# Kernel optimization log

Hardware: AMD Instinct MI355X
Metric: run time of the kernel (lower is better)

## Reference

```python
import jax, jax.numpy as jnp
import numpy as np

# 5x5 Sobel kernels (exact constants from the torch module)
_GX5 = np.array([[2.,1.,1e-6,-1.,-2.],[3.,2.,1e-6,-2.,-3.],[4.,3.,0.,-3.,-4.],[3.,2.,1e-6,-2.,-3.],[2.,1.,1e-6,-1.,-2.]], np.float32)
_GY5 = np.array([[2.,3.,4.,3.,2.],[1.,2.,3.,2.,1.],[1e-6,1e-6,1e-6,1e-6,1e-6],[-1.,-2.,-3.,-2.,-1.],[-2.,-3.,-4.,-3.,-2.]], np.float32)


def _sobel(x):  # x: [B,1,H,W] -> [B,2,H,W] (gx, gy)
    k = jnp.stack([jnp.asarray(_GX5), jnp.asarray(_GY5)])[:, None]  # [2,1,5,5]
    return jax.lax.conv_general_dilated(x, k, (1, 1), 'SAME',
                                        dimension_numbers=('NCHW', 'OIHW', 'NCHW'))


def _quantize(gx, gy):
    # OrientQuantize: magnitude + orientation quantized to 8 bins
    div = 3.1416 / 8.0
    mag = jnp.sqrt(gx * gx + gy * gy + 1e-8)
    o = jnp.arctan2(gy, gx)
    conds = [
        (o >= div) & (o < 3 * div),
        (o >= 3 * div) & (o < 5 * div),
        (o >= 5 * div) & (o < 7 * div),
        ((o >= 7 * div) & (o < 8 * div)) | ((o >= -8 * div) & (o < -7 * div)),
        (o >= -7 * div) & (o < -5 * div),
        (o >= -5 * div) & (o < -3 * div),
        (o >= -3 * div) & (o < -div),
        (o >= -div) & (o < div),
    ]
    q = jnp.select(conds, [jnp.full_like(o, float(i)) for i in range(8)], 3.0)
    return mag, q.astype(jnp.int32)


def setup_inputs() -> dict:
    key = jax.random.key(0)
    k1, k2, k3 = jax.random.split(key, 3)
    return {
        'seg_map': jax.random.normal(k1, (2, 21, 256, 256), jnp.float32),
        'dense_ft': jax.random.normal(k2, (2, 256, 256, 256), jnp.float32),
        'mask': jax.random.normal(k3, (2, 21, 256, 256), jnp.float32),
        'label_with_bg': jnp.ones((2, 21), jnp.float32),
    }


def reference(seg_map, dense_ft, mask, label_with_bg):
    BETA, K, STEP = 1000.0, 100, 5
    n, C, h, w = seg_map.shape
    nfg, ch, hw = C - 1, dense_ft.shape[1], h * w

    # ---- Mix_fg: per-class Sobel orientation edges on sharpened softmax ----
    seg = jax.nn.softmax(seg_map * BETA, axis=1)[:, 1:]            # [n,nfg,h,w]
    edges = _sobel(seg.reshape(n * nfg, 1, h, w)).reshape(n, nfg, 2, h, w)
    label_fg = label_with_bg[:, 1:]                                 # [n,nfg]
    edges = edges * label_fg[:, :, None, None, None]
    mag, q = _quantize(edges[:, :, 0], edges[:, :, 1])              # [n,nfg,h,w]

    # ---- boundary pixels: strongest-K edge magnitudes per (b,c) ----
    _, pos = jax.lax.top_k(mag.reshape(n, nfg, hw), K)              # [n,nfg,K]
    o = jnp.take_along_axis(q.reshape(n, nfg, hw), pos, -1) + 1     # 1..8

    # ---- in_out_div: walk STEP pixels along/against gradient orientation ----
    mod4 = ((o % 4) == 0).astype(jnp.int32)
    horiz = ((o == 2) | (o == 6)).astype(jnp.int32)
    p_out = jnp.where(o < 4, STEP * STEP, -STEP)   # (-STEP)**(1+(o<4))
    p_in = jnp.where(o < 4, -STEP, 1)              # (-STEP)**(o<4)
    s_out = jnp.where(o % 2 == 0, -1, 1)           # (-1)**(1+o)
    s_in = -s_out                                   # (-1)**o
    out_idx = pos + p_out * mod4 * w + s_out * horiz
    in_idx = pos + p_in * mod4 * w + s_in * horiz

    def valid(x):
        return (x % (w - 1) != 0) & (x % (w - 1) != 1) & (x > 0) & (x < hw - 1)

    v_out, v_in = valid(out_idx), valid(in_idx)                     # [n,nfg,K] bool
    oi = jnp.clip(out_idx, 0, hw - 1)
    ii = jnp.clip(in_idx, 0, hw - 1)

    # ---- gather features / mask probs at walked positions ----
    dense = jax.nn.softmax(dense_ft, axis=1).reshape(n, ch, hw)
    msk = jax.nn.softmax(mask, axis=1).reshape(n, C, hw)
    b = jnp.arange(n)[:, None, None]
    outs = dense[b, :, oi]                                          # [n,nfg,K,ch]
    ins = jax.lax.stop_gradient(dense[b, :, ii])                    # detached
    outs_m = jax.lax.stop_gradient(msk[b, :, oi])
    ins_m = jax.lax.stop_gradient(msk[b, :, ii])

    sim = jnp.einsum('bcie,bcje->bcij', outs, ins)                  # [n,nfg,K,K]
    sim_m = jnp.einsum('bcie,bcje->bcij', outs_m, ins_m)

    fvi = v_in.astype(sim.dtype)
    fvo = v_out.astype(sim.dtype)
    ci = jnp.maximum(fvi.sum(-1), 1.0)
    co = jnp.maximum(fvo.sum(-1), 1.0)

    def rowmean(s):  # mean over in-samples -> [n,nfg,K]
        return (s * fvi[:, :, None, :]).sum(-1) / ci[..., None]

    def colmean(s):  # mean over out-samples -> [n,nfg,K]
        return (s * fvo[:, :, :, None]).sum(-2) / co[..., None]

    def gmean(s):    # global masked mean -> [n,nfg]
        num = (s * fvo[:, :, :, None] * fvi[:, :, None, :]).sum((-2, -1))
        return num / jnp.maximum(fvo.sum(-1) * fvi.sum(-1), 1.0)

    def beacon(sgn_mask, sgn_dense, vals, v):
        # loss_constructor: signed masked means over FP/FN/TP/TN categories
        def term(cat, sign):
            m = (cat & v).astype(vals.dtype)
            cnt = m.sum(-1)
            return sign * jnp.where(cnt > 0, (vals * m).sum(-1) / jnp.maximum(cnt, 1.0), 0.0)
        FP = sgn_mask & ~sgn_dense
        FN = ~sgn_mask & sgn_dense
        TP = ~sgn_mask & ~sgn_dense
        TN = sgn_mask & sgn_dense
        return term(FP, -1.0) + term(FN, 1.0) + term(TP, 1.0) + term(TN, -1.0)

    g = gmean(sim)
    gm = gmean(sim_m)
    rm, rmm = rowmean(sim), rowmean(sim_m)
    cm, cmm = colmean(sim), colmean(sim_m)
    sgn_rm = jax.lax.stop_gradient(rm) > g[..., None]
    sgn_rmm = rmm > gm[..., None]
    sgn_cm = jax.lax.stop_gradient(cm) > g[..., None]
    sgn_cmm = cmm > gm[..., None]

    loss_bc = beacon(sgn_rmm, sgn_rm, rm, v_out) + beacon(sgn_cmm, sgn_cm, cm, v_in)
    gate = ((v_in.sum(-1) >= 10) & (v_out.sum(-1) >= 10)).astype(loss_bc.dtype)
    gate = gate * (label_fg > 0).astype(loss_bc.dtype)
    return (loss_bc * gate).sum()
```

## Files before the change

### kernel.cpp

```cpp
#include <hip/hip_runtime.h>
#include <math.h>

#define HW 65536
#define WID 256
#define HEI 256
#define NB 2
#define NFG 20
#define NMAP 40
#define CH 256
#define CSEG 21
#define TK 100
#define PARTS 32
#define PARTN (HW / PARTS)
#define RPP (HEI / PARTS)
#define CAND (PARTS * TK)
#define MCH 13

__device__ __constant__ float c_GX[25] = {
  2.f,1.f,1e-6f,-1.f,-2.f,
  3.f,2.f,1e-6f,-2.f,-3.f,
  4.f,3.f,0.f,-3.f,-4.f,
  3.f,2.f,1e-6f,-2.f,-3.f,
  2.f,1.f,1e-6f,-1.f,-2.f};
__device__ __constant__ float c_GY[25] = {
  2.f,3.f,4.f,3.f,2.f,
  1.f,2.f,3.f,2.f,1.f,
  1e-6f,1e-6f,1e-6f,1e-6f,1e-6f,
  -1.f,-2.f,-3.f,-2.f,-1.f,
  -2.f,-3.f,-4.f,-3.f,-2.f};

__global__ __launch_bounds__(256) void k_seg(const float* __restrict__ seg_map,
                                             double* __restrict__ seg) {
  int idx = blockIdx.x * blockDim.x + threadIdx.x;
  if (idx >= NB * HW) return;
  int b = idx / HW, p = idx % HW;
  double x[CSEG];
  double m = -INFINITY;
  #pragma unroll
  for (int c = 0; c < CSEG; ++c) {
    double v = (double)seg_map[(size_t)(b * CSEG + c) * HW + p] * 1000.0;
    x[c] = v;
    m = fmax(m, v);
  }
  double s = 0.0;
  #pragma unroll
  for (int c = 0; c < CSEG; ++c) {
    double d = x[c] - m;
    double e = (d < -746.0) ? 0.0 : exp(d);
    x[c] = e; s += e;
  }
  #pragma unroll
  for (int c = 1; c < CSEG; ++c)
    seg[(size_t)(b * NFG + (c - 1)) * HW + p] = x[c] / s;
}

__global__ __launch_bounds__(256) void k_sobel(
    const double* __restrict__ seg, const float* __restrict__ label,
    unsigned char* __restrict__ qb, unsigned long long* __restrict__ keys) {
  int mapi = blockIdx.x / PARTS, part = blockIdx.x % PARTS;
  int tid = threadIdx.x;
  int row0 = part * RPP;
  const double* im = seg + (size_t)mapi * HW;

  __shared__ double tile[RPP + 4][WID];

  for (int r = 0; r < RPP + 4; ++r) {
    int gr = row0 - 2 + r;
    tile[r][tid] = (gr >= 0 && gr < HEI) ? im[gr * WID + tid] : 0.0;
  }
  __syncthreads();

  int b = mapi / NFG, c = mapi % NFG;
  double lab = (double)label[b * CSEG + c + 1];
  const double DIVQ = 3.1416 / 8.0;
  double u1 = tan(DIVQ);
  double u3 = tan(3.0 * DIVQ);
  double w5 = tan(M_PI - 5.0 * DIVQ);
  double w7 = tan(M_PI - 7.0 * DIVQ);

  #pragma unroll
  for (int k = 0; k < RPP; ++k) {
    double gx = 0.0, gy = 0.0;
    #pragma unroll
    for (int dy = 0; dy < 5; ++dy) {
      #pragma unroll
      for (int dx = 0; dx < 5; ++dx) {
        int xx = tid + dx - 2;
        double v = (xx >= 0 && xx < WID) ? tile[k + dy][xx] : 0.0;
        gx += v * (double)c_GX[dy * 5 + dx];
        gy += v * (double)c_GY[dy * 5 + dx];
      }
    }
    gx *= lab; gy *= lab;
    double rad2 = gx * gx + gy * gy + 1e-8;
    int qv;
    if (gx > 0.0) {
      double t1 = u1 * gx, t3 = u3 * gx;
      if (gy >= t3) qv = 1;
      else if (gy >= t1) qv = 0;
      else if (gy >= -t1) qv = 7;
      else if (gy >= -t3) qv = 6;
      else qv = 5;
    } else if (gx < 0.0) {
      double ag = -gx;
      if (gy >= 0.0) {
        if (gy <= w7 * ag) qv = 3;
        else if (gy <= w5 * ag) qv = 2;
        else qv = 1;
      } else {
        double ay = -gy;
        if (ay < w7 * ag) qv = 3;
        else if (ay < w5 * ag) qv = 4;
        else qv = 5;
      }
    } else {
      if (gy > 0.0) qv = 1;
      else if (gy < 0.0) qv = 5;
      else qv = 7;
    }
    size_t gp = (size_t)mapi * HW + (size_t)(row0 + k) * WID + tid;
    keys[gp] = (unsigned long long)__double_as_longlong(rad2);
    qb[gp] = (unsigned char)qv;
  }
}

__global__ __launch_bounds__(256) void k_select(
    const unsigned long long* __restrict__ keys,
    unsigned long long* __restrict__ ckey, int* __restrict__ cidx) {
  int mapi = blockIdx.x / PARTS, part = blockIdx.x % PARTS;
  int tid = threadIdx.x;
  int lane = tid & 63, w = tid >> 6;
  const unsigned long long* kp = keys + (size_t)mapi * HW + (size_t)part * PARTN;

  __shared__ unsigned long long sk[PARTN];
  __shared__ unsigned int hist4[4][256];
  __shared__ int wtot[4];
  __shared__ int s_r, s_cnt, s_bsel, s_selcnt;
  __shared__ unsigned long long s_kv;

  unsigned long long mykey[RPP];
  #pragma unroll
  for (int k = 0; k < RPP; ++k) {
    unsigned long long key = kp[k * 256 + tid];
    mykey[k] = key;
    sk[k * 256 + tid] = key;
  }
  hist4[0][tid] = 0; hist4[1][tid] = 0; hist4[2][tid] = 0; hist4[3][tid] = 0;
  if (tid == 0) { s_r = TK; s_cnt = 0; }
  __syncthreads();

  unsigned long long pfx = 0ull, msk = 0ull;
  int early = 0;
  for (int round = 0; round < 8; ++round) {
    int shift = 56 - 8 * round;
    int curb = -1; unsigned int curc = 0;
    #pragma unroll
    for (int k = 0; k < RPP; ++k) {
      unsigned long long key = mykey[k];
      int bk = ((key & msk) == pfx) ? (int)((key >> shift) & 0xFF) : -1;
      if (bk == curb) { ++curc; }
      else {
        if (curb >= 0) atomicAdd(&hist4[w][curb], curc);
        curb = bk; curc = 1;
      }
    }
    if (curb >= 0) atomicAdd(&hist4[w][curb], curc);
    __syncthreads();
    int r = s_r;
    int cnt = (int)(hist4[0][tid] + hist4[1][tid] + hist4[2][tid] + hist4[3][tid]);
    hist4[0][tid] = 0; hist4[1][tid] = 0; hist4[2][tid] = 0; hist4[3][tid] = 0;
    int v = cnt;
    #pragma unroll
    for (int off = 1; off < 64; off <<= 1) {
      int u = __shfl_down(v, off, 64);
      if (lane + off < 64) v += u;
    }
    if (lane == 0) wtot[w] = v;
    __syncthreads();
    int add = 0;
    for (int ww = w + 1; ww < 4; ++ww) add += wtot[ww];
    v += add;
    if (v >= r && v - cnt < r) { s_bsel = tid; s_r = r - (v - cnt); s_selcnt = cnt; }
    __syncthreads();
    pfx |= ((unsigned long long)s_bsel << shift);
    msk |= (0xFFull << shift);
    if (s_selcnt == 1) { early = 1; break; }
  }
  if (early) {
    #pragma unroll
    for (int k = 0; k < RPP; ++k)
      if ((mykey[k] & msk) == pfx) s_kv = mykey[k];
    __syncthreads();
  } else {
    if (tid == 0) s_kv = pfx;
    __syncthreads();
  }
  unsigned long long kv = s_kv;
  int need_eq = s_r;

  unsigned long long* outk = ckey + (size_t)mapi * CAND + (size_t)part * TK;
  int* outi = cidx + (size_t)mapi * CAND + (size_t)part * TK;
  int gbase = part * PARTN;
  const int CHN = PARTN / 256;
  int base = tid * CHN;
  int myeq = 0;
  for (int k = 0; k < CHN; ++k) {
    unsigned long long key = sk[base + k];
    if (key > kv) {
      int slot = atomicAdd(&s_cnt, 1);
      outk[slot] = key; outi[slot] = gbase + base + k;
    } else if (key == kv) ++myeq;
  }
  int v2 = myeq;
  #pragma unroll
  for (int off = 1; off < 64; off <<= 1) {
    int u = __shfl_up(v2, off, 64);
    if (lane >= off) v2 += u;
  }
  if (lane == 63) wtot[w] = v2;
  __syncthreads();
  int addl = 0;
  for (int ww = 0; ww < w; ++ww) addl += wtot[ww];
  int incl = v2 + addl;
  int rank = incl - myeq;
  int eqtot = wtot[0] + wtot[1] + wtot[2] + wtot[3];
  int lo = eqtot - need_eq;
  int wb = TK - need_eq;
  for (int k = 0; k < CHN; ++k) {
    unsigned long long key = sk[base + k];
    if (key == kv) {
      if (rank >= lo) { outk[wb + rank - lo] = key; outi[wb + rank - lo] = gbase + base + k; }
      ++rank;
    }
  }
}

__global__ __launch_bounds__(256) void k_topk_merge(
    const unsigned long long* __restrict__ ckey,
    const int* __restrict__ cidx, int* __restrict__ pos) {
  int mapi = blockIdx.x, tid = threadIdx.x;
  int lane = tid & 63, w = tid >> 6;
  __shared__ unsigned long long k_[CAND];
  __shared__ int i_[CAND];
  __shared__ int eqi[CAND];
  __shared__ unsigned int hist4[4][256];
  __shared__ int wtot[4];
  __shared__ int s_r, s_cnt, s_eqn, s_bsel, s_selcnt, s_w2;
  __shared__ unsigned long long s_kv;
  for (int c = tid; c < CAND; c += 256) {
    k_[c] = ckey[(size_t)mapi * CAND + c];
    i_[c] = cidx[(size_t)mapi * CAND + c];
  }
  hist4[0][tid] = 0; hist4[1][tid] = 0; hist4[2][tid] = 0; hist4[3][tid] = 0;
  if (tid == 0) { s_r = TK; s_cnt = 0; s_eqn = 0; s_w2 = 0; }
  __syncthreads();
  unsigned long long pfx = 0ull, msk = 0ull;
  int early = 0;
  int mbase = tid * MCH;
  for (int round = 0; round < 8; ++round) {
    int shift = 56 - 8 * round;
    int curb = -1; unsigned int curc = 0;
    for (int t = 0; t < MCH; ++t) {
      int cc = mbase + t;
      int bk = -1;
      if (cc < CAND) {
        unsigned long long key = k_[cc];
        if ((key & msk) == pfx) bk = (int)((key >> shift) & 0xFF);
      }
      if (bk == curb) { ++curc; }
      else {
        if (curb >= 0) atomicAdd(&hist4[w][curb], curc);
        curb = bk; curc = 1;
      }
    }
    if (curb >= 0) atomicAdd(&hist4[w][curb], curc);
    __syncthreads();
    int r = s_r;
    int cnt = (int)(hist4[0][tid] + hist4[1][tid] + hist4[2][tid] + hist4[3][tid]);
    hist4[0][tid] = 0; hist4[1][tid] = 0; hist4[2][tid] = 0; hist4[3][tid] = 0;
    int v = cnt;
    #pragma unroll
    for (int off = 1; off < 64; off <<= 1) {
      int u = __shfl_down(v, off, 64);
      if (lane + off < 64) v += u;
    }
    if (lane == 0) wtot[w] = v;
    __syncthreads();
    int add = 0;
    for (int ww = w + 1; ww < 4; ++ww) add += wtot[ww];
    v += add;
    if (v >= r && v - cnt < r) { s_bsel = tid; s_r = r - (v - cnt); s_selcnt = cnt; }
    __syncthreads();
    pfx |= ((unsigned long long)s_bsel << shift);
    msk |= (0xFFull << shift);
    if (s_selcnt == 1) { early = 1; break; }
  }
  if (early) {
    for (int c = tid; c < CAND; c += 256)
      if ((k_[c] & msk) == pfx) s_kv = k_[c];
    __syncthreads();
  } else {
    if (tid == 0) s_kv = pfx;
    __syncthreads();
  }
  unsigned long long kv = s_kv;
  int need_eq = s_r;
  for (int c = tid; c < CAND; c += 256) {
    unsigned long long key = k_[c];
    if (key > kv) {
      int slot = atomicAdd(&s_cnt, 1);
      pos[mapi * TK + slot] = i_[c];
    } else if (key == kv) {
      int e = atomicAdd(&s_eqn, 1);
      eqi[e] = i_[c];
    }
  }
  __syncthreads();
  int eqn = s_eqn;
  int wb = TK - need_eq;
  if (eqn == need_eq) {
    for (int e = tid; e < eqn; e += 256) pos[mapi * TK + wb + e] = eqi[e];
    return;
  }
  if (tid == 0) s_r = need_eq;
  __syncthreads();
  unsigned int ipfx = 0u, imsk = 0u;
  for (int round = 0; round < 2; ++round) {
    int shift = 8 * (1 - round);
    for (int e = tid; e < eqn; e += 256) {
      unsigned int iv = (unsigned int)eqi[e];
      if ((iv & imsk) == ipfx)
        atomicAdd(&hist4[w][(iv >> shift) & 0xFFu], 1u);
    }
    __syncthreads();
    int r = s_r;
    int cnt = (int)(hist4[0][tid] + hist4[1][tid] + hist4[2][tid] + hist4[3][tid]);
    hist4[0][tid] = 0; hist4[1][tid] = 0; hist4[2][tid] = 0; hist4[3][tid] = 0;
    int v = cnt;
    #pragma unroll
    for (int off = 1; off < 64; off <<= 1) {
      int u = __shfl_down(v, off, 64);
      if (lane + off < 64) v += u;
    }
    if (lane == 0) wtot[w] = v;
    __syncthreads();
    int add = 0;
    for (int ww = w + 1; ww < 4; ++ww) add += wtot[ww];
    v += add;
    if (v >= r && v - cnt < r) { s_bsel = tid; s_r = r - (v - cnt); }
    __syncthreads();
    ipfx |= ((unsigned int)s_bsel << shift);
    imsk |= (0xFFu << shift);
  }
  int thrIdx = (int)ipfx;
  for (int e = tid; e < eqn; e += 256) {
    if (eqi[e] >= thrIdx) {
      int slot = atomicAdd(&s_w2, 1);
      pos[mapi * TK + wb + slot] = eqi[e];
    }
  }
}

__global__ __launch_bounds__(256) void k_gather(
    const float* __restrict__ dense_ft, const float* __restrict__ maskp,
    const unsigned char* __restrict__ qb, const int* __restrict__ pos,
    double* __restrict__ outs, double* __restrict__ ins,
    double* __restrict__ outs_m, double* __restrict__ ins_m,
    int* __restrict__ voutArr, int* __restrict__ vinArr) {
  int blk = blockIdx.x;
  int mapi = blk / TK, j = blk % TK;
  int b = mapi / NFG;
  int tid = threadIdx.x;
  int lane = tid & 63, w = tid >> 6;
  int p = pos[mapi * TK + j];
  int o = (int)qb[(size_t)mapi * HW + p] + 1;
  int mod4 = ((o & 3) == 0) ? 1 : 0;
  int horiz = (o == 2 || o == 6) ? 1 : 0;
  int po = (o < 4) ? 25 : -5;
  int pi = (o < 4) ? -5 : 1;
  int so = ((o & 1) == 0) ? -1 : 1;
  int si = -so;
  int out_idx = p + po * mod4 * WID + so * horiz;
  int in_idx  = p + pi * mod4 * WID + si * horiz;
  int ro = out_idx % 255; if (ro < 0) ro += 255;
  int ri = in_idx  % 255; if (ri < 0) ri += 255;
  int vo = (ro != 0 && ro != 1 && out_idx > 0 && out_idx < HW - 1) ? 1 : 0;
  int vi = (ri != 0 && ri != 1 && in_idx  > 0 && in_idx  < HW - 1) ? 1 : 0;
  int oi = out_idx < 0 ? 0 : (out_idx > HW - 1 ? HW - 1 : out_idx);
  int ii = in_idx  < 0 ? 0 : (in_idx  > HW - 1 ? HW - 1 : in_idx);
  if (tid == 0) { voutArr[mapi * TK + j] = vo; vinArr[mapi * TK + j] = vi; }

  if (w < 2) {
    int idx = (w == 0) ? oi : ii;
    double x[4];
    double mx = -INFINITY;
    #pragma unroll
    for (int q = 0; q < 4; ++q) {
      x[q] = (double)dense_ft[(size_t)(b * CH + lane + 64 * q) * HW + idx];
      mx = fmax(mx, x[q]);
    }
    #pragma unroll
    for (int off = 1; off < 64; off <<= 1) mx = fmax(mx, __shfl_xor(mx, off, 64));
    double e[4], s = 0.0;
    #pragma unroll
    for (int q = 0; q < 4; ++q) { e[q] = exp(x[q] - mx); s += e[q]; }
    #pragma unroll
    for (int off = 1; off < 64; off <<= 1) s += __shfl_xor(s, off, 64);
    double* dst = ((w == 0) ? outs : ins) + ((size_t)mapi * TK + j) * CH;
    #pragma unroll
    for (int q = 0; q < 4; ++q) dst[lane + 64 * q] = e[q] / s;
  } else {
    int idx = (w == 2) ? oi : ii;
    double y = (lane < CSEG) ? (double)maskp[(size_t)(b * CSEG + lane) * HW + idx]
                             : -INFINITY;
    double mx = y;
    #pragma unroll
    for (int off = 1; off < 64; off <<= 1) mx = fmax(mx, __shfl_xor(mx, off, 64));
    double e = (lane < CSEG) ? exp(y - mx) : 0.0;
    double s = e;
    #pragma unroll
    for (int off = 1; off < 64; off <<= 1) s += __shfl_xor(s, off, 64);
    if (lane < CSEG)
      (((w == 2) ? outs_m : ins_m) + ((size_t)mapi * TK + j) * CSEG)[lane] = e / s;
  }
}

__global__ __launch_bounds__(256) void k_stats(
    const double* __restrict__ outs, const double* __restrict__ ins,
    const double* __restrict__ outs_m, const double* __restrict__ ins_m,
    const int* __restrict__ voutArr, const int* __restrict__ vinArr,
    const float* __restrict__ label, double* __restrict__ lossmap) {
  int mapi = blockIdx.x, tid = threadIdx.x;
  int b = mapi / NFG, c = mapi % NFG;
  __shared__ double fvo[TK], fvi[TK];
  __shared__ double avi[CH], avo[CH], avim[CSEG], avom[CSEG];
  __shared__ double rm[TK], cm[TK], rmm[TK], cmm[TK];
  __shared__ double s_sfvo, s_sfvi;
  if (tid < TK) {
    fvo[tid] = (double)voutArr[mapi * TK + tid];
    fvi[tid] = (double)vinArr[mapi * TK + tid];
  }
  __syncthreads();
  if (tid == 0) {
    double a = 0.0, d = 0.0;
    for (int j2 = 0; j2 < TK; ++j2) { a += fvo[j2]; d += fvi[j2]; }
    s_sfvo = a; s_sfvi = d;
  }
  const double* OUT  = outs   + (size_t)mapi * TK * CH;
  const double* IN   = ins    + (size_t)mapi * TK * CH;
  const double* OUTm = outs_m + (size_t)mapi * TK * CSEG;
  const double* INm  = ins_m  + (size_t)mapi * TK * CSEG;
  {
    double a = 0.0, d = 0.0;
    for (int j2 = 0; j2 < TK; ++j2) {
      a += IN[j2 * CH + tid] * fvi[j2];
      d += OUT[j2 * CH + tid] * fvo[j2];
    }
    avi[tid] = a; avo[tid] = d;
  }
  if (tid < CSEG) {
    double a = 0.0, d = 0.0;
    for (int j2 = 0; j2 < TK; ++j2) {
      a += INm[j2 * CSEG + tid] * fvi[j2];
      d += OUTm[j2 * CSEG + tid] * fvo[j2];
    }
    avim[tid] = a; avom[tid] = d;
  }
  __syncthreads();
  double ci = fmax(s_sfvi, 1.0), co = fmax(s_sfvo, 1.0);
  if (tid < TK) {
    double d1 = 0.0, d2 = 0.0, d3 = 0.0, d4 = 0.0;
    for (int e = 0; e < CH; ++e) { d1 += OUT[tid * CH + e] * avi[e]; d2 += IN[tid * CH + e] * avo[e]; }
    for (int e = 0; e < CSEG; ++e) { d3 += OUTm[tid * CSEG + e] * avim[e]; d4 += INm[tid * CSEG + e] * avom[e]; }
    rm[tid] = d1 / ci; cm[tid] = d2 / co; rmm[tid] = d3 / ci; cmm[tid] = d4 / co;
  }
  __syncthreads();
  if (tid == 0) {
    double g = 0.0, gm = 0.0;
    for (int e = 0; e < CH; ++e) g += avo[e] * avi[e];
    for (int e = 0; e < CSEG; ++e) gm += avom[e] * avim[e];
    double den = fmax(s_sfvo * s_sfvi, 1.0);
    g /= den; gm /= den;
    double loss = 0.0;
    {
      double s[4] = {0, 0, 0, 0}, cn[4] = {0, 0, 0, 0};
      for (int j2 = 0; j2 < TK; ++j2) {
        int smv = rmm[j2] > gm;
        int dmv = rm[j2] > g;
        int cat = smv ? (dmv ? 3 : 0) : (dmv ? 1 : 2);
        s[cat] += rm[j2] * fvo[j2];
        cn[cat] += fvo[j2];
      }
      const double sg[4] = {-1.0, 1.0, 1.0, -1.0};
      for (int t = 0; t < 4; ++t)
        if (cn[t] > 0.0) loss += sg[t] * (s[t] / fmax(cn[t], 1.0));
    }
    {
      double s[4] = {0, 0, 0, 0}, cn[4] = {0, 0, 0, 0};
      for (int j2 = 0; j2 < TK; ++j2) {
        int smv = cmm[j2] > gm;
        int dmv = cm[j2] > g;
        int cat = smv ? (dmv ? 3 : 0) : (dmv ? 1 : 2);
        s[cat] += cm[j2] * fvi[j2];
        cn[cat] += fvi[j2];
      }
      const double sg[4] = {-1.0, 1.0, 1.0, -1.0};
      for (int t = 0; t < 4; ++t)
        if (cn[t] > 0.0) loss += sg[t] * (s[t] / fmax(cn[t], 1.0));
    }
    float lab = label[b * CSEG + c + 1];
    double gate = (s_sfvi >= 10.0 && s_sfvo >= 10.0 && lab > 0.f) ? 1.0 : 0.0;
    lossmap[mapi] = loss * gate;
  }
}

__global__ __launch_bounds__(64) void k_final(const double* __restrict__ lossmap,
                                              float* __restrict__ out) {
  if (threadIdx.x == 0 && blockIdx.x == 0) {
    double s = 0.0;
    for (int i = 0; i < NMAP; ++i) s += lossmap[i];
    out[0] = (float)s;
  }
}

extern "C" void kernel_launch(void* const* d_in, const int* in_sizes, int n_in,
                              void* d_out, int out_size, void* d_ws, size_t ws_size,
                              hipStream_t stream) {
  const float* seg_map  = (const float*)d_in[0];
  const float* dense_ft = (const float*)d_in[1];
  const float* maskp    = (const float*)d_in[2];
  const float* label    = (const float*)d_in[3];
  float* outp = (float*)d_out;

  char* w = (char*)d_ws;
  double* seg = (double*)w;               w += (size_t)NB * NFG * HW * 8;
  unsigned long long* keys = (unsigned long long*)w; w += (size_t)NMAP * HW * 8;
  double* outs   = (double*)w;            w += (size_t)NMAP * TK * CH * 8;
  double* ins    = (double*)w;            w += (size_t)NMAP * TK * CH * 8;
  double* outs_m = (double*)w;            w += (size_t)NMAP * TK * CSEG * 8;
  double* ins_m  = (double*)w;            w += (size_t)NMAP * TK * CSEG * 8;
  double* lossmap = (double*)w;           w += (size_t)NMAP * 8;
  unsigned long long* ckey = (unsigned long long*)w; w += (size_t)NMAP * CAND * 8;
  int* cidx = (int*)w;                    w += (size_t)NMAP * CAND * 4;
  int* pos  = (int*)w;                    w += (size_t)NMAP * TK * 4;
  int* vout = (int*)w;                    w += (size_t)NMAP * TK * 4;
  int* vin  = (int*)w;                    w += (size_t)NMAP * TK * 4;
  unsigned char* qb = (unsigned char*)w;  w += (size_t)NMAP * HW;

  k_seg<<<(NB * HW + 255) / 256, 256, 0, stream>>>(seg_map, seg);
  k_sobel<<<NMAP * PARTS, 256, 0, stream>>>(seg, label, qb, keys);
  k_select<<<NMAP * PARTS, 256, 0, stream>>>(keys, ckey, cidx);
  k_topk_merge<<<NMAP, 256, 0, stream>>>(ckey, cidx, pos);
  k_gather<<<NMAP * TK, 256, 0, stream>>>(dense_ft, maskp, qb, pos, outs, ins,
                                          outs_m, ins_m, vout, vin);
  k_stats<<<NMAP, 256, 0, stream>>>(outs, ins, outs_m, ins_m, vout, vin, label, lossmap);
  k_final<<<1, 64, 0, stream>>>(lossmap, outp);
}
```

Measured before the change: 176.0 us.

## Fuse channel softmax into Sobel kernel and drop intermediate seg buffer

Removes the separate softmax kernel and the fp64 seg buffer it wrote. Each Sobel block now computes the 21-channel sharpened softmax for its tile rows plus halo directly from seg_map and keeps only the needed class. This avoids one launch and a round-trip of the double-precision seg array through memory. In exchange, every one of the 40 maps recomputes the full 21-channel fp64 exp softmax, with halo rows on top, so exp work and seg_map reads grow by roughly 30x.

```diff
diff --git a/kernel.cpp b/kernel.cpp
--- a/kernel.cpp
+++ b/kernel.cpp
@@ -29,48 +29,42 @@
   -1.f,-2.f,-3.f,-2.f,-1.f,
   -2.f,-3.f,-4.f,-3.f,-2.f};
 
-__global__ __launch_bounds__(256) void k_seg(const float* __restrict__ seg_map,
-                                             double* __restrict__ seg) {
-  int idx = blockIdx.x * blockDim.x + threadIdx.x;
-  if (idx >= NB * HW) return;
-  int b = idx / HW, p = idx % HW;
-  double x[CSEG];
-  double m = -INFINITY;
-  #pragma unroll
-  for (int c = 0; c < CSEG; ++c) {
-    double v = (double)seg_map[(size_t)(b * CSEG + c) * HW + p] * 1000.0;
-    x[c] = v;
-    m = fmax(m, v);
-  }
-  double s = 0.0;
-  #pragma unroll
-  for (int c = 0; c < CSEG; ++c) {
-    double d = x[c] - m;
-    double e = (d < -746.0) ? 0.0 : exp(d);
-    x[c] = e; s += e;
-  }
-  #pragma unroll
-  for (int c = 1; c < CSEG; ++c)
-    seg[(size_t)(b * NFG + (c - 1)) * HW + p] = x[c] / s;
-}
-
 __global__ __launch_bounds__(256) void k_sobel(
-    const double* __restrict__ seg, const float* __restrict__ label,
+    const float* __restrict__ seg_map, const float* __restrict__ label,
     unsigned char* __restrict__ qb, unsigned long long* __restrict__ keys) {
   int mapi = blockIdx.x / PARTS, part = blockIdx.x % PARTS;
   int tid = threadIdx.x;
   int row0 = part * RPP;
-  const double* im = seg + (size_t)mapi * HW;
+  int b = mapi / NFG, c = mapi % NFG;
 
   __shared__ double tile[RPP + 4][WID];
 
   for (int r = 0; r < RPP + 4; ++r) {
     int gr = row0 - 2 + r;
-    tile[r][tid] = (gr >= 0 && gr < HEI) ? im[gr * WID + tid] : 0.0;
-  }
-  __syncthreads();
-
-  int b = mapi / NFG, c = mapi % NFG;
+    double val = 0.0;
+    if (gr >= 0 && gr < HEI) {
+      int p = gr * WID + tid;
+      double x[CSEG];
+      double m = -INFINITY;
+      #pragma unroll
+      for (int ch = 0; ch < CSEG; ++ch) {
+        double v = (double)seg_map[(size_t)(b * CSEG + ch) * HW + p] * 1000.0;
+        x[ch] = v;
+        m = fmax(m, v);
+      }
+      double s = 0.0;
+      #pragma unroll
+      for (int ch = 0; ch < CSEG; ++ch) {
+        double d = x[ch] - m;
+        double e = (d < -746.0) ? 0.0 : exp(d);
+        x[ch] = e; s += e;
+      }
+      val = x[c + 1] / s;
+    }
+    tile[r][tid] = val;
+  }
+  __syncthreads();
+
   double lab = (double)label[b * CSEG + c + 1];
   const double DIVQ = 3.1416 / 8.0;
   double u1 = tan(DIVQ);
@@ -533,7 +527,6 @@
   float* outp = (float*)d_out;
 
   char* w = (char*)d_ws;
-  double* seg = (double*)w;               w += (size_t)NB * NFG * HW * 8;
   unsigned long long* keys = (unsigned long long*)w; w += (size_t)NMAP * HW * 8;
   double* outs   = (double*)w;            w += (size_t)NMAP * TK * CH * 8;
   double* ins    = (double*)w;            w += (size_t)NMAP * TK * CH * 8;
@@ -547,8 +540,7 @@
   int* vin  = (int*)w;                    w += (size_t)NMAP * TK * 4;
   unsigned char* qb = (unsigned char*)w;  w += (size_t)NMAP * HW;
 
-  k_seg<<<(NB * HW + 255) / 256, 256, 0, stream>>>(seg_map, seg);
-  k_sobel<<<NMAP * PARTS, 256, 0, stream>>>(seg, label, qb, keys);
+  k_sobel<<<NMAP * PARTS, 256, 0, stream>>>(seg_map, label, qb, keys);
   k_select<<<NMAP * PARTS, 256, 0, stream>>>(keys, ckey, cidx);
   k_topk_merge<<<NMAP, 256, 0, stream>>>(ckey, cidx, pos);
   k_gather<<<NMAP * TK, 256, 0, stream>>>(dense_ft, maskp, qb, pos, outs, ins,
```

After: 318.0 us. 80.7% more time.
